# Optimization experiments

Hardware: AMD Instinct MI355X
Metric: run time of the kernel (lower is better)

Reference implementation:

```python
import jax, jax.numpy as jnp
import numpy as np
import math

N, S, T, D = 4, 2048, 2048, 1024

def setup_inputs() -> dict:
    key = jax.random.key(0)
    ks = jax.random.split(key, 6)
    scale = 1.0 / math.sqrt(D)
    return {
        "query": jax.random.normal(ks[0], (N, S, D), dtype=jnp.float32),
        "key": jax.random.normal(ks[1], (N, T, D), dtype=jnp.float32),
        "value": jax.random.normal(ks[2], (N, T, D), dtype=jnp.float32),
        # causal mask: 1 = attend, 0 = masked out (masked_fill where mask == 0)
        "attn_mask": jnp.tril(jnp.ones((S, T), dtype=jnp.int32)),
        "Wq": jax.random.normal(ks[3], (D, D), dtype=jnp.float32) * scale,
        "Wk": jax.random.normal(ks[4], (D, D), dtype=jnp.float32) * scale,
        "Wv": jax.random.normal(ks[5], (D, D), dtype=jnp.float32) * scale,
    }

def reference(query, key, value, attn_mask, Wq, Wk, Wv):
    # nn.Linear(bias=False): y = x @ W.T
    q = jnp.einsum('nsd,ed->nse', query, Wq)
    k = jnp.einsum('ntd,ed->nte', key, Wk)
    v = jnp.einsum('ntd,ed->nte', value, Wv)
    # scaled dot-product scores [N, S, T]
    dot = jnp.einsum('nse,nte->nst', q, k) / jnp.sqrt(jnp.asarray(D, q.dtype))
    dot = jnp.where(attn_mask == 0, -jnp.inf, dot)
    scores = jax.nn.softmax(dot, axis=-1)
    # dropout is identity in eval mode
    y = jnp.einsum('nst,nte->nse', scores, v)
    return y
```

## Files before the change

kernel.cpp:

```cpp
#include <hip/hip_runtime.h>
#include <math.h>

using u16 = unsigned short;
typedef __attribute__((ext_vector_type(8))) __bf16 bf16x8;
typedef __attribute__((ext_vector_type(4))) float f32x4;
typedef __attribute__((ext_vector_type(4))) float f4v;
typedef __attribute__((ext_vector_type(8))) u16 u16x8;

__device__ __forceinline__ u16 f2bf(float f) {
  unsigned u = __float_as_uint(f);
  u += 0x7fffu + ((u >> 16) & 1u);
  return (u16)(u >> 16);
}

__device__ __forceinline__ void gload16(const void* g, void* l) {
  __builtin_amdgcn_global_load_lds(
      (const __attribute__((address_space(1))) unsigned int*)g,
      (__attribute__((address_space(3))) unsigned int*)l, 16, 0, 0);
}

__device__ __forceinline__ f32x4 MF(bf16x8 a, bf16x8 b, f32x4 c) {
  return __builtin_amdgcn_mfma_f32_16x16x32_bf16(a, b, c, 0, 0, 0);
}

__device__ __forceinline__ bf16x8 pk8(f4v a, f4v b) {
  bf16x8 x;
  x[0] = (__bf16)a[0]; x[1] = (__bf16)a[1]; x[2] = (__bf16)a[2]; x[3] = (__bf16)a[3];
  x[4] = (__bf16)b[0]; x[5] = (__bf16)b[1]; x[6] = (__bf16)b[2]; x[7] = (__bf16)b[3];
  return x;
}

__global__ __launch_bounds__(256) void cast3_f32_bf16(
    const float* __restrict__ p0, const float* __restrict__ p1,
    const float* __restrict__ p2, u16* __restrict__ out, size_t ostride) {
  int z = blockIdx.z;
  const float* in = (z == 0) ? p0 : (z == 1) ? p1 : p2;
  size_t i = ((size_t)blockIdx.x * 256 + threadIdx.x) * 8;
  f4v a = *reinterpret_cast<const f4v*>(in + i);
  f4v b = *reinterpret_cast<const f4v*>(in + i + 4);
  u16x8 r;
  r[0] = f2bf(a[0]); r[1] = f2bf(a[1]); r[2] = f2bf(a[2]); r[3] = f2bf(a[3]);
  r[4] = f2bf(b[0]); r[5] = f2bf(b[1]); r[6] = f2bf(b[2]); r[7] = f2bf(b[3]);
  *reinterpret_cast<u16x8*>(out + z * ostride + i) = r;
}

__global__ __launch_bounds__(256) void transpose_bf16k(const u16* __restrict__ in,
                                                       u16* __restrict__ out) {
  __shared__ u16 t[64][65];
  int c0 = blockIdx.x * 64, r0 = blockIdx.y * 64;
  size_t zb = (size_t)blockIdx.z * 2048 * 1024;
  const u16* I = in + zb;
  u16* O = out + zb;
  int tx = threadIdx.x & 63, ty = threadIdx.x >> 6;
  #pragma unroll
  for (int i = 0; i < 64; i += 4)
    t[ty + i][tx] = I[(size_t)(r0 + ty + i) * 1024 + c0 + tx];
  __syncthreads();
  #pragma unroll
  for (int i = 0; i < 64; i += 4)
    O[(size_t)(c0 + ty + i) * 2048 + r0 + tx] = t[tx][ty + i];
}

__global__ __launch_bounds__(256) void proj_fused(
    const float* __restrict__ Aq, const float* __restrict__ Ak,
    const float* __restrict__ Av, const u16* __restrict__ W,
    u16* __restrict__ Qp, u16* __restrict__ Kp, u16* __restrict__ Vp) {
  int h = blockIdx.x;
  int l = (h & 7) * 192 + (h >> 3);
  int bn = l & 7;
  int bm192 = l >> 3;
  int which = bm192 >> 6;
  int bm = bm192 & 63;
  const float* Ag = ((which == 0) ? Aq : (which == 1) ? Ak : Av) +
                    (size_t)bm * 128 * 1024;
  const u16* Bg = W + (size_t)which * 1048576 + (size_t)bn * 128 * 1024;
  u16* Cg = (which == 0) ? Qp : (which == 1) ? Kp : Vp;

  __shared__ __align__(16) u16 As[2][128 * 32];
  __shared__ __align__(16) u16 Bs[2][128 * 32];

  const int tid = threadIdx.x, lane = tid & 63, wave = tid >> 6;
  const int wr = wave >> 1, wc = wave & 1;
  const int fr = lane & 15, kq = (lane >> 4) * 8;

  const float* ag0 = Ag + (size_t)(tid >> 2) * 1024 + (tid & 3) * 8;
  const float* ag1 = ag0 + 64 * 1024;
  const int w0i = (tid >> 2) * 32 + (tid & 3) * 8;
  const int w1i = w0i + 2048;
  const int ch0 = wave, ch1 = wave + 4;
  const int e0 = ch0 * 512 + lane * 8, e1 = ch1 * 512 + lane * 8;
  const int br0 = e0 >> 5, bc0 = e0 & 31, br1 = e1 >> 5, bc1 = e1 & 31;
  const u16* b0 = Bg + (size_t)br0 * 1024 + bc0;
  const u16* b1 = Bg + (size_t)br1 * 1024 + bc1;

  f32x4 acc[4][4] = {};
  f4v pc0, pc1, pc2, pc3, pn0, pn1, pn2, pn3;

  gload16(b0, &Bs[0][ch0 * 512]);
  gload16(b1, &Bs[0][ch1 * 512]);
  pc0 = *(const f4v*)(ag0);      pc1 = *(const f4v*)(ag0 + 4);
  pc2 = *(const f4v*)(ag1);      pc3 = *(const f4v*)(ag1 + 4);
  pn0 = *(const f4v*)(ag0 + 32); pn1 = *(const f4v*)(ag0 + 36);
  pn2 = *(const f4v*)(ag1 + 32); pn3 = *(const f4v*)(ag1 + 36);
  *(bf16x8*)&As[0][w0i] = pk8(pc0, pc1);
  *(bf16x8*)&As[0][w1i] = pk8(pc2, pc3);
  pc0 = pn0; pc1 = pn1; pc2 = pn2; pc3 = pn3;
  asm volatile("s_waitcnt vmcnt(4)" ::: "memory");
  asm volatile("s_waitcnt lgkmcnt(0)" ::: "memory");
  __builtin_amdgcn_s_barrier();

  for (int t = 0; t < 32; ++t) {
    const int cur = t & 1;
    if (t < 31) {
      const int k0 = (t + 1) * 32;
      gload16(b0 + k0, &Bs[cur ^ 1][ch0 * 512]);
      gload16(b1 + k0, &Bs[cur ^ 1][ch1 * 512]);
    }
    if (t < 30) {
      const float* ap0 = ag0 + (t + 2) * 32;
      const float* ap1 = ag1 + (t + 2) * 32;
      pn0 = *(const f4v*)(ap0); pn1 = *(const f4v*)(ap0 + 4);
      pn2 = *(const f4v*)(ap1); pn3 = *(const f4v*)(ap1 + 4);
    }
    bf16x8 af[4], bfv[4];
    #pragma unroll
    for (int m = 0; m < 4; ++m)
      af[m] = *reinterpret_cast<const bf16x8*>(&As[cur][(wr * 64 + m * 16 + fr) * 32 + kq]);
    #pragma unroll
    for (int n = 0; n < 4; ++n)
      bfv[n] = *reinterpret_cast<const bf16x8*>(&Bs[cur][(wc * 64 + n * 16 + fr) * 32 + kq]);
    #pragma unroll
    for (int m = 0; m < 4; ++m)
      #pragma unroll
      for (int n = 0; n < 4; ++n)
        acc[m][n] = MF(af[m], bfv[n], acc[m][n]);
    if (t < 31) {
      *(bf16x8*)&As[cur ^ 1][w0i] = pk8(pc0, pc1);
      *(bf16x8*)&As[cur ^ 1][w1i] = pk8(pc2, pc3);
      pc0 = pn0; pc1 = pn1; pc2 = pn2; pc3 = pn3;
      if (t < 30) { asm volatile("s_waitcnt vmcnt(4)" ::: "memory"); }
      else        { asm volatile("s_waitcnt vmcnt(0)" ::: "memory"); }
      asm volatile("s_waitcnt lgkmcnt(0)" ::: "memory");
      __builtin_amdgcn_s_barrier();
    }
  }

  const int row0 = bm * 128 + wr * 64 + (lane >> 4) * 4;
  const int col0 = bn * 128 + wc * 64 + fr;
  #pragma unroll
  for (int m = 0; m < 4; ++m)
    #pragma unroll
    for (int n = 0; n < 4; ++n)
      #pragma unroll
      for (int j = 0; j < 4; ++j)
        Cg[(size_t)(row0 + m * 16 + j) * 1024 + (col0 + n * 16)] = f2bf(acc[m][n][j]);
}

#define BM 128
#define BN 128
#define BK 32

template<typename OutT, int MODE>
__global__ __launch_bounds__(256) void gemm_bt(
    const u16* __restrict__ A, const u16* __restrict__ B, OutT* __restrict__ C,
    int K, int lda, int ldb, int ldc,
    size_t sA, size_t sB, size_t sC, float alpha) {
  int bn, bm, bz;
  int kEnd = K;
  if (MODE == 1) {
    int h = blockIdx.x;
    int l = (h & 7) * 68 + (h >> 3);
    bz = l / 136;
    int t = l % 136;
    bm = (int)((sqrtf(8.f * (float)t + 1.f) - 1.f) * 0.5f);
    while ((bm + 1) * (bm + 2) / 2 <= t) ++bm;
    while (bm * (bm + 1) / 2 > t) --bm;
    bn = t - bm * (bm + 1) / 2;
  } else {
    int l = blockIdx.x;
    bm = 15 - (l >> 5);
    int rest = l & 31;
    bz = rest >> 3;
    bn = rest & 7;
    kEnd = (K < (bm + 1) * BM) ? K : (bm + 1) * BM;
  }
  const u16* Ag = A + sA * bz + (size_t)bm * BM * lda;
  const u16* Bg = B + sB * bz + (size_t)bn * BN * ldb;
  OutT* Cg = C + sC * bz;

  __shared__ __align__(16) u16 As[2][BM * BK];
  __shared__ __align__(16) u16 Bs[2][BN * BK];

  const int tid = threadIdx.x;
  const int lane = tid & 63, wave = tid >> 6;
  const int wr = wave >> 1, wc = wave & 1;

  const int ch0 = wave, ch1 = wave + 4;
  const int e0 = ch0 * 512 + lane * 8, e1 = ch1 * 512 + lane * 8;
  const int r0 = e0 >> 5, c0 = e0 & 31, r1 = e1 >> 5, c1 = e1 & 31;
  const u16* a0 = Ag + (size_t)r0 * lda + c0;
  const u16* a1 = Ag + (size_t)r1 * lda + c1;
  const u16* b0 = Bg + (size_t)r0 * ldb + c0;
  const u16* b1 = Bg + (size_t)r1 * ldb + c1;

  f32x4 acc[4][4] = {};

  const int fr = lane & 15, kq = (lane >> 4) * 8;
  const int nt = kEnd / BK;

  gload16(a0, &As[0][ch0 * 512]);
  gload16(a1, &As[0][ch1 * 512]);
  gload16(b0, &Bs[0][ch0 * 512]);
  gload16(b1, &Bs[0][ch1 * 512]);
  __syncthreads();

  for (int t = 0; t < nt; ++t) {
    const int cur = t & 1;
    if (t + 1 < nt) {
      const int k0 = (t + 1) * BK;
      gload16(a0 + k0, &As[cur ^ 1][ch0 * 512]);
      gload16(a1 + k0, &As[cur ^ 1][ch1 * 512]);
      gload16(b0 + k0, &Bs[cur ^ 1][ch0 * 512]);
      gload16(b1 + k0, &Bs[cur ^ 1][ch1 * 512]);
    }
    bf16x8 af[4], bfv[4];
    #pragma unroll
    for (int m = 0; m < 4; ++m)
      af[m] = *reinterpret_cast<const bf16x8*>(&As[cur][(wr * 64 + m * 16 + fr) * BK + kq]);
    #pragma unroll
    for (int n = 0; n < 4; ++n)
      bfv[n] = *reinterpret_cast<const bf16x8*>(&Bs[cur][(wc * 64 + n * 16 + fr) * BK + kq]);
    #pragma unroll
    for (int m = 0; m < 4; ++m)
      #pragma unroll
      for (int n = 0; n < 4; ++n)
        acc[m][n] = MF(af[m], bfv[n], acc[m][n]);
    __syncthreads();
  }

  const int row0 = bm * BM + wr * 64 + (lane >> 4) * 4;
  const int col0 = bn * BN + wc * 64 + fr;
  #pragma unroll
  for (int m = 0; m < 4; ++m)
    #pragma unroll
    for (int n = 0; n < 4; ++n) {
      #pragma unroll
      for (int j = 0; j < 4; ++j) {
        float val = acc[m][n][j] * alpha;
        size_t idx = (size_t)(row0 + m * 16 + j) * ldc + (col0 + n * 16);
        if constexpr (sizeof(OutT) == 2) Cg[idx] = f2bf(val);
        else Cg[idx] = val;
      }
    }
}

__global__ __launch_bounds__(256) void softmax_causal(float* __restrict__ sc) {
  int r = blockIdx.x;
  int s = r & 2047;
  float* row = sc + (size_t)r * 2048;
  int tid = threadIdx.x;
  int t0 = tid * 8;
  f4v x0 = {-1e30f, -1e30f, -1e30f, -1e30f};
  f4v x1 = {-1e30f, -1e30f, -1e30f, -1e30f};
  if (t0 <= s)     x0 = reinterpret_cast<const f4v*>(row)[tid * 2];
  if (t0 + 4 <= s) x1 = reinterpret_cast<const f4v*>(row)[tid * 2 + 1];
  float v[8] = {x0[0], x0[1], x0[2], x0[3], x1[0], x1[1], x1[2], x1[3]};
  float mx = -1e30f;
  #pragma unroll
  for (int j = 0; j < 8; ++j) {
    v[j] = ((t0 + j) <= s) ? v[j] : -1e30f;
    mx = fmaxf(mx, v[j]);
  }
  #pragma unroll
  for (int o = 32; o; o >>= 1) mx = fmaxf(mx, __shfl_xor(mx, o, 64));
  __shared__ float red[8];
  if ((tid & 63) == 0) red[tid >> 6] = mx;
  __syncthreads();
  mx = fmaxf(fmaxf(red[0], red[1]), fmaxf(red[2], red[3]));
  float p[8];
  float sum = 0.f;
  #pragma unroll
  for (int j = 0; j < 8; ++j) {
    p[j] = ((t0 + j) <= s) ? __expf(v[j] - mx) : 0.f;
    sum += p[j];
  }
  #pragma unroll
  for (int o = 32; o; o >>= 1) sum += __shfl_xor(sum, o, 64);
  if ((tid & 63) == 0) red[4 + (tid >> 6)] = sum;
  __syncthreads();
  sum = red[4] + red[5] + red[6] + red[7];
  float inv = 1.0f / sum;
  u16x8 o8;
  #pragma unroll
  for (int j = 0; j < 8; ++j) o8[j] = f2bf(p[j] * inv);
  if (t0 <= (s | 127))
    reinterpret_cast<u16x8*>(row)[tid] = o8;
}

extern "C" void kernel_launch(void* const* d_in, const int* in_sizes, int n_in,
                              void* d_out, int out_size, void* d_ws, size_t ws_size,
                              hipStream_t stream) {
  const float* q  = (const float*)d_in[0];
  const float* k  = (const float*)d_in[1];
  const float* v  = (const float*)d_in[2];
  const float* Wq = (const float*)d_in[4];
  const float* Wk = (const float*)d_in[5];
  const float* Wv = (const float*)d_in[6];
  float* out = (float*)d_out;
  char* ws = (char*)d_ws;

  const size_t MB = 1024ull * 1024ull;
  float* sc = (float*)ws;
  u16* Vp  = (u16*)(ws + 0 * MB);
  u16* wqb = (u16*)(ws + 16 * MB);
  u16* Vt  = (u16*)(ws + 64 * MB);
  u16* Kp  = (u16*)(ws + 80 * MB);
  u16* Qp  = (u16*)(ws + 96 * MB);
  (void)in_sizes; (void)n_in; (void)out_size; (void)ws_size;

  cast3_f32_bf16<<<dim3(512, 1, 3), 256, 0, stream>>>(Wq, Wk, Wv, wqb, 1048576);

  proj_fused<<<1536, 256, 0, stream>>>(q, k, v, wqb, Qp, Kp, Vp);

  transpose_bf16k<<<dim3(16, 32, 4), 256, 0, stream>>>(Vp, Vt);

  gemm_bt<float, 1><<<544, 256, 0, stream>>>(
      Qp, Kp, sc, 1024, 1024, 1024, 2048,
      (size_t)2048 * 1024, (size_t)2048 * 1024, (size_t)2048 * 2048, 0.03125f);

  softmax_causal<<<8192, 256, 0, stream>>>(sc);

  gemm_bt<float, 2><<<512, 256, 0, stream>>>(
      (u16*)ws, Vt, out, 2048, 4096, 2048, 1024,
      (size_t)2048 * 4096, (size_t)1024 * 2048, (size_t)2048 * 1024, 1.0f);
}
```

Before: 180.7 us.

## Fold Wk into the query projection and store attention scores as bf16

Reassociates the score product as q·(Wq^T Wk)·k^T. A small 1024×1024 weight GEMM runs first, and the raw keys are only cast to bf16, so the key projection GEMM over all tokens disappears. The score matrix is now written and read as bf16 in place instead of fp32, which halves score traffic for the softmax and PV GEMM. This adds a transpose-cast kernel and extra launches, and brings extra bf16 rounding in the fused weight and in the stored scores.

```diff
diff --git a/kernel.cpp b/kernel.cpp
--- a/kernel.cpp
+++ b/kernel.cpp
@@ -11,6 +11,10 @@
   unsigned u = __float_as_uint(f);
   u += 0x7fffu + ((u >> 16) & 1u);
   return (u16)(u >> 16);
+}
+__device__ __forceinline__ float bf2f(u16 b) {
+  unsigned u = ((unsigned)b) << 16;
+  return __uint_as_float(u);
 }
 
 __device__ __forceinline__ void gload16(const void* g, void* l) {
@@ -44,6 +48,24 @@
   *reinterpret_cast<u16x8*>(out + z * ostride + i) = r;
 }
 
+__global__ __launch_bounds__(256) void tcast_w(
+    const float* __restrict__ wk, const float* __restrict__ wq,
+    u16* __restrict__ wkT, u16* __restrict__ wqT) {
+  __shared__ float t[64][65];
+  int z = blockIdx.z;
+  const float* I = z ? wq : wk;
+  u16* O = z ? wqT : wkT;
+  int c0 = blockIdx.x * 64, r0 = blockIdx.y * 64;
+  int tx = threadIdx.x & 63, ty = threadIdx.x >> 6;
+  #pragma unroll
+  for (int i = 0; i < 64; i += 4)
+    t[ty + i][tx] = I[(size_t)(r0 + ty + i) * 1024 + c0 + tx];
+  __syncthreads();
+  #pragma unroll
+  for (int i = 0; i < 64; i += 4)
+    O[(size_t)(c0 + ty + i) * 1024 + r0 + tx] = f2bf(t[tx][ty + i]);
+}
+
 __global__ __launch_bounds__(256) void transpose_bf16k(const u16* __restrict__ in,
                                                        u16* __restrict__ out) {
   __shared__ u16 t[64][65];
@@ -62,19 +84,18 @@
 }
 
 __global__ __launch_bounds__(256) void proj_fused(
-    const float* __restrict__ Aq, const float* __restrict__ Ak,
-    const float* __restrict__ Av, const u16* __restrict__ W,
-    u16* __restrict__ Qp, u16* __restrict__ Kp, u16* __restrict__ Vp) {
+    const float* __restrict__ Aq, const float* __restrict__ Av,
+    const u16* __restrict__ W,
+    u16* __restrict__ Yq, u16* __restrict__ Vp) {
   int h = blockIdx.x;
-  int l = (h & 7) * 192 + (h >> 3);
+  int l = (h & 7) * 128 + (h >> 3);
   int bn = l & 7;
-  int bm192 = l >> 3;
-  int which = bm192 >> 6;
-  int bm = bm192 & 63;
-  const float* Ag = ((which == 0) ? Aq : (which == 1) ? Ak : Av) +
-                    (size_t)bm * 128 * 1024;
+  int bm128 = l >> 3;
+  int which = bm128 >> 6;
+  int bm = bm128 & 63;
+  const float* Ag = (which == 0 ? Aq : Av) + (size_t)bm * 128 * 1024;
   const u16* Bg = W + (size_t)which * 1048576 + (size_t)bn * 128 * 1024;
-  u16* Cg = (which == 0) ? Qp : (which == 1) ? Kp : Vp;
+  u16* Cg = (which == 0) ? Yq : Vp;
 
   __shared__ __align__(16) u16 As[2][128 * 32];
   __shared__ __align__(16) u16 Bs[2][128 * 32];
@@ -165,9 +186,12 @@
     const u16* __restrict__ A, const u16* __restrict__ B, OutT* __restrict__ C,
     int K, int lda, int ldb, int ldc,
     size_t sA, size_t sB, size_t sC, float alpha) {
-  int bn, bm, bz;
+  int bn, bm, bz = 0;
   int kEnd = K;
-  if (MODE == 1) {
+  if (MODE == 0) {
+    bm = blockIdx.x >> 3;
+    bn = blockIdx.x & 7;
+  } else if (MODE == 1) {
     int h = blockIdx.x;
     int l = (h & 7) * 68 + (h >> 3);
     bz = l / 136;
@@ -254,21 +278,19 @@
     }
 }
 
-__global__ __launch_bounds__(256) void softmax_causal(float* __restrict__ sc) {
+__global__ __launch_bounds__(256) void softmax_causal(u16* __restrict__ sc) {
   int r = blockIdx.x;
   int s = r & 2047;
-  float* row = sc + (size_t)r * 2048;
+  u16* row = sc + (size_t)r * 2048;
   int tid = threadIdx.x;
   int t0 = tid * 8;
-  f4v x0 = {-1e30f, -1e30f, -1e30f, -1e30f};
-  f4v x1 = {-1e30f, -1e30f, -1e30f, -1e30f};
-  if (t0 <= s)     x0 = reinterpret_cast<const f4v*>(row)[tid * 2];
-  if (t0 + 4 <= s) x1 = reinterpret_cast<const f4v*>(row)[tid * 2 + 1];
-  float v[8] = {x0[0], x0[1], x0[2], x0[3], x1[0], x1[1], x1[2], x1[3]};
+  u16x8 raw = {0, 0, 0, 0, 0, 0, 0, 0};
+  if (t0 <= s) raw = *reinterpret_cast<const u16x8*>(row + t0);
+  float v[8];
   float mx = -1e30f;
   #pragma unroll
   for (int j = 0; j < 8; ++j) {
-    v[j] = ((t0 + j) <= s) ? v[j] : -1e30f;
+    v[j] = ((t0 + j) <= s) ? bf2f(raw[j]) : -1e30f;
     mx = fmaxf(mx, v[j]);
   }
   #pragma unroll
@@ -294,7 +316,7 @@
   #pragma unroll
   for (int j = 0; j < 8; ++j) o8[j] = f2bf(p[j] * inv);
   if (t0 <= (s | 127))
-    reinterpret_cast<u16x8*>(row)[tid] = o8;
+    *reinterpret_cast<u16x8*>(row + t0) = o8;
 }
 
 extern "C" void kernel_launch(void* const* d_in, const int* in_sizes, int n_in,
@@ -310,27 +332,35 @@
   char* ws = (char*)d_ws;
 
   const size_t MB = 1024ull * 1024ull;
-  float* sc = (float*)ws;
-  u16* Vp  = (u16*)(ws + 0 * MB);
-  u16* wqb = (u16*)(ws + 16 * MB);
-  u16* Vt  = (u16*)(ws + 64 * MB);
-  u16* Kp  = (u16*)(ws + 80 * MB);
-  u16* Qp  = (u16*)(ws + 96 * MB);
+  u16* sc   = (u16*)ws;
+  u16* Vp   = (u16*)(ws + 0 * MB);
+  u16* wkT  = (u16*)(ws + 16 * MB);
+  u16* wqT  = (u16*)(ws + 18 * MB);
+  u16* wsl  = (u16*)(ws + 20 * MB);
+  u16* Xkbf = (u16*)(ws + 32 * MB);
+  u16* Vt   = (u16*)(ws + 48 * MB);
+  u16* Yq   = (u16*)(ws + 64 * MB);
   (void)in_sizes; (void)n_in; (void)out_size; (void)ws_size;
 
-  cast3_f32_bf16<<<dim3(512, 1, 3), 256, 0, stream>>>(Wq, Wk, Wv, wqb, 1048576);
-
-  proj_fused<<<1536, 256, 0, stream>>>(q, k, v, wqb, Qp, Kp, Vp);
+  tcast_w<<<dim3(16, 16, 2), 256, 0, stream>>>(Wk, Wq, wkT, wqT);
+  cast3_f32_bf16<<<dim3(512, 1, 1), 256, 0, stream>>>(Wv, nullptr, nullptr,
+                                                      wsl + 1048576, 0);
+  cast3_f32_bf16<<<dim3(4096, 1, 1), 256, 0, stream>>>(k, nullptr, nullptr, Xkbf, 0);
+
+  gemm_bt<u16, 0><<<64, 256, 0, stream>>>(
+      wkT, wqT, wsl, 1024, 1024, 1024, 1024, 0, 0, 0, 1.0f);
+
+  proj_fused<<<1024, 256, 0, stream>>>(q, v, wsl, Yq, Vp);
 
   transpose_bf16k<<<dim3(16, 32, 4), 256, 0, stream>>>(Vp, Vt);
 
-  gemm_bt<float, 1><<<544, 256, 0, stream>>>(
-      Qp, Kp, sc, 1024, 1024, 1024, 2048,
+  gemm_bt<u16, 1><<<544, 256, 0, stream>>>(
+      Yq, Xkbf, sc, 1024, 1024, 1024, 2048,
       (size_t)2048 * 1024, (size_t)2048 * 1024, (size_t)2048 * 2048, 0.03125f);
 
   softmax_causal<<<8192, 256, 0, stream>>>(sc);
 
   gemm_bt<float, 2><<<512, 256, 0, stream>>>(
-      (u16*)ws, Vt, out, 2048, 4096, 2048, 1024,
-      (size_t)2048 * 4096, (size_t)1024 * 2048, (size_t)2048 * 1024, 1.0f);
-}
+      sc, Vt, out, 2048, 2048, 2048, 1024,
+      (size_t)2048 * 2048, (size_t)1024 * 2048, (size_t)2048 * 1024, 1.0f);
+}
```

Result: slower. 192.7 us (+6.6%).

## Store attention scores in bf16 and use 8-wave GEMM blocks

Applied to the files above, without the earlier changes.

The QK^T GEMM now writes its scaled scores as bf16 instead of fp32. Softmax reads and writes those bf16 rows in place, and the PV GEMM reads them with a compact 2048 stride. The GEMM kernel moves from 4 to 8 waves per block, each wave computing a 64x32 sub-tile, to raise occupancy and cut per-wave register pressure. Together these halve the score-matrix traffic, at the cost of rounding the pre-softmax logits to bf16.

```diff
diff --git a/kernel.cpp b/kernel.cpp
--- a/kernel.cpp
+++ b/kernel.cpp
@@ -11,6 +11,10 @@
   unsigned u = __float_as_uint(f);
   u += 0x7fffu + ((u >> 16) & 1u);
   return (u16)(u >> 16);
+}
+__device__ __forceinline__ float bf2f(u16 b) {
+  unsigned u = ((unsigned)b) << 16;
+  return __uint_as_float(u);
 }
 
 __device__ __forceinline__ void gload16(const void* g, void* l) {
@@ -156,12 +160,8 @@
         Cg[(size_t)(row0 + m * 16 + j) * 1024 + (col0 + n * 16)] = f2bf(acc[m][n][j]);
 }
 
-#define BM 128
-#define BN 128
-#define BK 32
-
 template<typename OutT, int MODE>
-__global__ __launch_bounds__(256) void gemm_bt(
+__global__ __launch_bounds__(512) void gemm_bt8(
     const u16* __restrict__ A, const u16* __restrict__ B, OutT* __restrict__ C,
     int K, int lda, int ldb, int ldc,
     size_t sA, size_t sB, size_t sC, float alpha) {
@@ -182,68 +182,60 @@
     int rest = l & 31;
     bz = rest >> 3;
     bn = rest & 7;
-    kEnd = (K < (bm + 1) * BM) ? K : (bm + 1) * BM;
-  }
-  const u16* Ag = A + sA * bz + (size_t)bm * BM * lda;
-  const u16* Bg = B + sB * bz + (size_t)bn * BN * ldb;
+    kEnd = (K < (bm + 1) * 128) ? K : (bm + 1) * 128;
+  }
+  const u16* Ag = A + sA * bz + (size_t)bm * 128 * lda;
+  const u16* Bg = B + sB * bz + (size_t)bn * 128 * ldb;
   OutT* Cg = C + sC * bz;
 
-  __shared__ __align__(16) u16 As[2][BM * BK];
-  __shared__ __align__(16) u16 Bs[2][BN * BK];
+  __shared__ __align__(16) u16 As[2][128 * 32];
+  __shared__ __align__(16) u16 Bs[2][128 * 32];
 
   const int tid = threadIdx.x;
-  const int lane = tid & 63, wave = tid >> 6;
-  const int wr = wave >> 1, wc = wave & 1;
-
-  const int ch0 = wave, ch1 = wave + 4;
-  const int e0 = ch0 * 512 + lane * 8, e1 = ch1 * 512 + lane * 8;
-  const int r0 = e0 >> 5, c0 = e0 & 31, r1 = e1 >> 5, c1 = e1 & 31;
+  const int lane = tid & 63, wv = tid >> 6;
+  const int wr = wv >> 2, wc = wv & 3;
+  const int fr = lane & 15, kq = (lane >> 4) * 8;
+
+  const int e0 = wv * 512 + lane * 8;
+  const int r0 = e0 >> 5, c0 = e0 & 31;
   const u16* a0 = Ag + (size_t)r0 * lda + c0;
-  const u16* a1 = Ag + (size_t)r1 * lda + c1;
   const u16* b0 = Bg + (size_t)r0 * ldb + c0;
-  const u16* b1 = Bg + (size_t)r1 * ldb + c1;
-
-  f32x4 acc[4][4] = {};
-
-  const int fr = lane & 15, kq = (lane >> 4) * 8;
-  const int nt = kEnd / BK;
-
-  gload16(a0, &As[0][ch0 * 512]);
-  gload16(a1, &As[0][ch1 * 512]);
-  gload16(b0, &Bs[0][ch0 * 512]);
-  gload16(b1, &Bs[0][ch1 * 512]);
+
+  f32x4 acc[4][2] = {};
+  const int nt = kEnd / 32;
+
+  gload16(a0, &As[0][wv * 512]);
+  gload16(b0, &Bs[0][wv * 512]);
   __syncthreads();
 
   for (int t = 0; t < nt; ++t) {
     const int cur = t & 1;
     if (t + 1 < nt) {
-      const int k0 = (t + 1) * BK;
-      gload16(a0 + k0, &As[cur ^ 1][ch0 * 512]);
-      gload16(a1 + k0, &As[cur ^ 1][ch1 * 512]);
-      gload16(b0 + k0, &Bs[cur ^ 1][ch0 * 512]);
-      gload16(b1 + k0, &Bs[cur ^ 1][ch1 * 512]);
-    }
-    bf16x8 af[4], bfv[4];
+      const int k0 = (t + 1) * 32;
+      gload16(a0 + k0, &As[cur ^ 1][wv * 512]);
+      gload16(b0 + k0, &Bs[cur ^ 1][wv * 512]);
+    }
+    bf16x8 af[4], bfv[2];
     #pragma unroll
     for (int m = 0; m < 4; ++m)
-      af[m] = *reinterpret_cast<const bf16x8*>(&As[cur][(wr * 64 + m * 16 + fr) * BK + kq]);
-    #pragma unroll
-    for (int n = 0; n < 4; ++n)
-      bfv[n] = *reinterpret_cast<const bf16x8*>(&Bs[cur][(wc * 64 + n * 16 + fr) * BK + kq]);
+      af[m] = *reinterpret_cast<const bf16x8*>(&As[cur][(wr * 64 + m * 16 + fr) * 32 + kq]);
+    #pragma unroll
+    for (int n = 0; n < 2; ++n)
+      bfv[n] = *reinterpret_cast<const bf16x8*>(&Bs[cur][(wc * 32 + n * 16 + fr) * 32 + kq]);
     #pragma unroll
     for (int m = 0; m < 4; ++m)
       #pragma unroll
-      for (int n = 0; n < 4; ++n)
+      for (int n = 0; n < 2; ++n)
         acc[m][n] = MF(af[m], bfv[n], acc[m][n]);
     __syncthreads();
   }
 
-  const int row0 = bm * BM + wr * 64 + (lane >> 4) * 4;
-  const int col0 = bn * BN + wc * 64 + fr;
+  const int row0 = bm * 128 + wr * 64 + (lane >> 4) * 4;
+  const int col0 = bn * 128 + wc * 32 + fr;
   #pragma unroll
   for (int m = 0; m < 4; ++m)
     #pragma unroll
-    for (int n = 0; n < 4; ++n) {
+    for (int n = 0; n < 2; ++n) {
       #pragma unroll
       for (int j = 0; j < 4; ++j) {
         float val = acc[m][n][j] * alpha;
@@ -254,21 +246,19 @@
     }
 }
 
-__global__ __launch_bounds__(256) void softmax_causal(float* __restrict__ sc) {
+__global__ __launch_bounds__(256) void softmax_causal(u16* __restrict__ sc) {
   int r = blockIdx.x;
   int s = r & 2047;
-  float* row = sc + (size_t)r * 2048;
+  u16* row = sc + (size_t)r * 2048;
   int tid = threadIdx.x;
   int t0 = tid * 8;
-  f4v x0 = {-1e30f, -1e30f, -1e30f, -1e30f};
-  f4v x1 = {-1e30f, -1e30f, -1e30f, -1e30f};
-  if (t0 <= s)     x0 = reinterpret_cast<const f4v*>(row)[tid * 2];
-  if (t0 + 4 <= s) x1 = reinterpret_cast<const f4v*>(row)[tid * 2 + 1];
-  float v[8] = {x0[0], x0[1], x0[2], x0[3], x1[0], x1[1], x1[2], x1[3]};
+  u16x8 raw = {0, 0, 0, 0, 0, 0, 0, 0};
+  if (t0 <= s) raw = *reinterpret_cast<const u16x8*>(row + t0);
+  float v[8];
   float mx = -1e30f;
   #pragma unroll
   for (int j = 0; j < 8; ++j) {
-    v[j] = ((t0 + j) <= s) ? v[j] : -1e30f;
+    v[j] = ((t0 + j) <= s) ? bf2f(raw[j]) : -1e30f;
     mx = fmaxf(mx, v[j]);
   }
   #pragma unroll
@@ -294,7 +284,7 @@
   #pragma unroll
   for (int j = 0; j < 8; ++j) o8[j] = f2bf(p[j] * inv);
   if (t0 <= (s | 127))
-    reinterpret_cast<u16x8*>(row)[tid] = o8;
+    *reinterpret_cast<u16x8*>(row + t0) = o8;
 }
 
 extern "C" void kernel_launch(void* const* d_in, const int* in_sizes, int n_in,
@@ -310,12 +300,12 @@
   char* ws = (char*)d_ws;
 
   const size_t MB = 1024ull * 1024ull;
-  float* sc = (float*)ws;
-  u16* Vp  = (u16*)(ws + 0 * MB);
-  u16* wqb = (u16*)(ws + 16 * MB);
-  u16* Vt  = (u16*)(ws + 64 * MB);
-  u16* Kp  = (u16*)(ws + 80 * MB);
-  u16* Qp  = (u16*)(ws + 96 * MB);
+  u16* sc   = (u16*)ws;
+  u16* Vp   = (u16*)(ws + 0 * MB);
+  u16* wqb  = (u16*)(ws + 16 * MB);
+  u16* Vt   = (u16*)(ws + 64 * MB);
+  u16* Kp   = (u16*)(ws + 80 * MB);
+  u16* Qp   = (u16*)(ws + 96 * MB);
   (void)in_sizes; (void)n_in; (void)out_size; (void)ws_size;
 
   cast3_f32_bf16<<<dim3(512, 1, 3), 256, 0, stream>>>(Wq, Wk, Wv, wqb, 1048576);
@@ -324,13 +314,13 @@
 
   transpose_bf16k<<<dim3(16, 32, 4), 256, 0, stream>>>(Vp, Vt);
 
-  gemm_bt<float, 1><<<544, 256, 0, stream>>>(
+  gemm_bt8<u16, 1><<<544, 512, 0, stream>>>(
       Qp, Kp, sc, 1024, 1024, 1024, 2048,
       (size_t)2048 * 1024, (size_t)2048 * 1024, (size_t)2048 * 2048, 0.03125f);
 
   softmax_causal<<<8192, 256, 0, stream>>>(sc);
 
-  gemm_bt<float, 2><<<512, 256, 0, stream>>>(
-      (u16*)ws, Vt, out, 2048, 4096, 2048, 1024,
-      (size_t)2048 * 4096, (size_t)1024 * 2048, (size_t)2048 * 1024, 1.0f);
-}
+  gemm_bt8<float, 2><<<512, 512, 0, stream>>>(
+      sc, Vt, out, 2048, 2048, 2048, 1024,
+      (size_t)2048 * 2048, (size_t)1024 * 2048, (size_t)2048 * 1024, 1.0f);
+}
```

Measured after the change: 170.9 us. -5.4%, faster.
